# Optimization experiments

Hardware: AMD Instinct MI355X
Metric: run time of the kernel (lower is better)

Reference implementation:

```python
import jax, jax.numpy as jnp
import numpy as np

NEG_SLOPE = 0.2  # PyG GATConv default leaky_relu negative slope

N_NODES = 10000
N_EDGES = 80000
IN_FEAT = 200
HID = 400
IN_HEADS = 8
OUT_FEAT = 200


def setup_inputs() -> dict:
    key = jax.random.key(0)
    ks = jax.random.split(key, 12)
    input_data = jax.random.normal(ks[0], (N_NODES, IN_FEAT), dtype=jnp.float32)
    edge_index = jax.random.randint(ks[1], (2, N_EDGES), 0, N_NODES, dtype=jnp.int64)
    # conv1: GATConv(200 -> 400, heads=8, concat=True)
    W1 = jax.random.normal(ks[2], (IN_FEAT, IN_HEADS * HID), dtype=jnp.float32) * 0.05
    a_src1 = jax.random.normal(ks[3], (IN_HEADS, HID), dtype=jnp.float32) * 0.05
    a_dst1 = jax.random.normal(ks[4], (IN_HEADS, HID), dtype=jnp.float32) * 0.05
    b1 = jnp.zeros((IN_HEADS * HID,), dtype=jnp.float32)
    # conv2: GATConv(3200 -> 200, heads=1, concat=False)
    W2 = jax.random.normal(ks[5], (IN_HEADS * HID, 1 * OUT_FEAT), dtype=jnp.float32) * 0.05
    a_src2 = jax.random.normal(ks[6], (1, OUT_FEAT), dtype=jnp.float32) * 0.05
    a_dst2 = jax.random.normal(ks[7], (1, OUT_FEAT), dtype=jnp.float32) * 0.05
    b2 = jnp.zeros((OUT_FEAT,), dtype=jnp.float32)
    return {"input_data": input_data, "edge_index": edge_index,
            "W1": W1, "a_src1": a_src1, "a_dst1": a_dst1, "b1": b1,
            "W2": W2, "a_src2": a_src2, "a_dst2": a_dst2, "b2": b2}


def _gat_conv(x, src, dst, W, a_src, a_dst, b, heads, out_ch, concat):
    """PyG GATConv (v1 attention), eval mode (no dropout)."""
    n = x.shape[0]
    h = (x @ W).reshape(n, heads, out_ch)              # [N,H,C]
    al_s = jnp.sum(h * a_src, axis=-1)                 # [N,H]
    al_d = jnp.sum(h * a_dst, axis=-1)                 # [N,H]
    e = jax.nn.leaky_relu(al_s[src] + al_d[dst], NEG_SLOPE)  # [E,H]
    # segment softmax over edges sharing the same destination node
    e_max = jax.ops.segment_max(e, dst, num_segments=n)       # [N,H]
    e_exp = jnp.exp(e - e_max[dst])                            # [E,H]
    denom = jax.ops.segment_sum(e_exp, dst, num_segments=n)   # [N,H]
    alpha = e_exp / denom[dst]                                 # [E,H]
    msg = h[src] * alpha[:, :, None]                           # [E,H,C]
    out = jax.ops.segment_sum(msg, dst, num_segments=n)       # [N,H,C]
    out = out.reshape(n, heads * out_ch) if concat else out.mean(axis=1)
    return out + b


def reference(input_data, edge_index, W1, a_src1, a_dst1, b1, W2, a_src2, a_dst2, b2):
    n = input_data.shape[0]
    loop = jnp.arange(n, dtype=edge_index.dtype)
    src = jnp.concatenate([edge_index[0], loop])  # add self-loops (PyG default)
    dst = jnp.concatenate([edge_index[1], loop])
    # eval mode: F.dropout is identity
    x = _gat_conv(input_data, src, dst, W1, a_src1, a_dst1, b1, IN_HEADS, HID, True)
    x = jax.nn.elu(x)
    x = _gat_conv(x, src, dst, W2, a_src2, a_dst2, b2, 1, OUT_FEAT, False)
    return x
```

## Files before the change

### kernel.cpp

```cpp
#include <hip/hip_runtime.h>
#include <math.h>

#define N_NODES 10000
#define N_EDGES 80000
#define ET (N_EDGES + N_NODES)
#define IN_FEAT 200
#define HID 400
#define NH1 8
#define F1 (NH1 * HID)
#define OUT_FEAT 200
#define NEG_SLOPE 0.2f

#define M_PAD 10048
#define K1 224
#define HSL (NH1 * K1)
#define XH_K 416
#define C1P 448
#define KALL (NH1 * XH_K)
#define N2P2 256
#define XHS 456

typedef __attribute__((ext_vector_type(8))) short short8_t;
typedef __attribute__((ext_vector_type(4))) float f32x4;


__device__ inline void edge_sd(const int* __restrict__ ei, int e, int& s, int& d) {
    if (e < N_EDGES) { s = ei[e]; d = ei[N_EDGES + e]; }
    else { s = e - N_EDGES; d = s; }
}

__device__ inline unsigned short f2bf(float x) {
    unsigned u = __float_as_uint(x);
    unsigned r = u + 0x7FFFu + ((u >> 16) & 1u);
    return (unsigned short)(r >> 16);
}

#define W1N (NH1 * C1P * K1)
#define W2N (N2P2 * KALL)
__global__ __launch_bounds__(256) void prep_w(const float* __restrict__ W1,
                                              const float* __restrict__ W2,
                                              unsigned short* __restrict__ W1f,
                                              unsigned short* __restrict__ W2f) {
    int idx = blockIdx.x * blockDim.x + threadIdx.x;
    if (idx < W1N) {
        int e    = idx & 7;
        int lane = (idx >> 3) & 63;
        int rem  = idx >> 9;
        int ks   = rem % 7;
        int jgh  = rem / 7;
        int jg   = jgh % 28;
        int h    = jgh / 28;
        int c = jg * 16 + (lane & 15);
        int k = ks * 32 + (lane >> 4) * 8 + e;
        float v = (k < IN_FEAT && c < HID) ? W1[(size_t)k * F1 + h * HID + c] : 0.f;
        W1f[idx] = f2bf(v);
    } else if (idx < W1N + W2N) {
        int t    = idx - W1N;
        int e    = t & 7;
        int lane = (t >> 3) & 63;
        int rem  = t >> 9;
        int ks   = rem % 13;
        int cgh  = rem / 13;
        int cg   = cgh % 16;
        int h    = cgh / 16;
        int c = cg * 16 + (lane & 15);
        int k = ks * 32 + (lane >> 4) * 8 + e;
        float v = (c < OUT_FEAT && k < HID) ? W2[(size_t)(h * HID + k) * OUT_FEAT + c] : 0.f;
        W2f[t] = f2bf(v);
    }
}

__global__ __launch_bounds__(256) void pvec_k(const float* __restrict__ W1,
                                              const float* __restrict__ a_src,
                                              const float* __restrict__ a_dst,
                                              float* __restrict__ p_src,
                                              float* __restrict__ p_dst) {
    int idx = blockIdx.x * blockDim.x + threadIdx.x;
    if (idx >= 2 * NH1 * IN_FEAT) return;
    int which = idx / (NH1 * IN_FEAT);
    int r = idx - which * (NH1 * IN_FEAT);
    int h = r / IN_FEAT, k = r - h * IN_FEAT;
    const float* av = (which == 0 ? a_src : a_dst) + h * HID;
    const float* wrow = W1 + (size_t)k * F1 + h * HID;
    float acc = 0.f;
    for (int c = 0; c < HID; ++c) acc += wrow[c] * av[c];
    (which == 0 ? p_src : p_dst)[h * IN_FEAT + k] = acc;
}

__global__ __launch_bounds__(512) void att1x(const float* __restrict__ X,
                                             const float* __restrict__ p_src,
                                             const float* __restrict__ p_dst,
                                             float* __restrict__ als,
                                             float* __restrict__ ald) {
    const int n    = blockIdx.x;
    const int head = threadIdx.x >> 6;
    const int lane = threadIdx.x & 63;
    const float* xp = X + (size_t)n * IN_FEAT;
    const float* ps = p_src + head * IN_FEAT;
    const float* pd = p_dst + head * IN_FEAT;
    float ss = 0.f, sd = 0.f;
    for (int k = lane; k < IN_FEAT; k += 64) {
        float v = xp[k];
        ss += v * ps[k];
        sd += v * pd[k];
    }
    for (int off = 32; off; off >>= 1) {
        ss += __shfl_down(ss, off);
        sd += __shfl_down(sd, off);
    }
    if (lane == 0) { als[n * NH1 + head] = ss; ald[n * NH1 + head] = sd; }
}

__global__ __launch_bounds__(256) void count_k(const int* __restrict__ ei, int* __restrict__ counts) {
    int e = blockIdx.x * blockDim.x + threadIdx.x;
    if (e >= ET) return;
    int s, d; edge_sd(ei, e, s, d);
    atomicAdd(&counts[d], 1);
}

__global__ __launch_bounds__(1024) void scan_k(const int* __restrict__ counts, int* __restrict__ offs) {
    __shared__ int part[1024];
    const int tid = threadIdx.x;
    const int base = tid * 10;
    int loc[10];
    int s = 0;
    for (int i = 0; i < 10; ++i) {
        int idx = base + i;
        int c = (idx < N_NODES) ? counts[idx] : 0;
        loc[i] = s; s += c;
    }
    part[tid] = s;
    __syncthreads();
    for (int off = 1; off < 1024; off <<= 1) {
        int v = (tid >= off) ? part[tid - off] : 0;
        __syncthreads();
        part[tid] += v;
        __syncthreads();
    }
    int pre = (tid > 0) ? part[tid - 1] : 0;
    for (int i = 0; i < 10; ++i) {
        int idx = base + i;
        if (idx < N_NODES) offs[idx] = pre + loc[i];
    }
    if (tid == 1023) offs[N_NODES] = part[1023];
}

__global__ __launch_bounds__(256) void scatter_k(const int* __restrict__ ei,
                                                 const int* __restrict__ offs,
                                                 int* __restrict__ cursor,
                                                 int* __restrict__ esrc) {
    int e = blockIdx.x * blockDim.x + threadIdx.x;
    if (e >= ET) return;
    int s, d; edge_sd(ei, e, s, d);
    int pos = atomicAdd(&cursor[d], 1);
    esrc[offs[d] + pos] = s;
}

__global__ __launch_bounds__(512) void agg1x(const float* __restrict__ X,
                                             const float* __restrict__ als1,
                                             const float* __restrict__ ald1,
                                             const int* __restrict__ offs,
                                             const int* __restrict__ esrc,
                                             unsigned short* __restrict__ xaggb) {
    __shared__ unsigned short sb[8][HSL];
    const int wave = threadIdx.x >> 6;
    const int lane = threadIdx.x & 63;
    const int n = blockIdx.x * 8 + wave;

    if (n < N_NODES) {
        float acc[NH1][4];
#pragma unroll
        for (int h = 0; h < NH1; ++h)
#pragma unroll
            for (int g = 0; g < 4; ++g) acc[h][g] = 0.f;

        const int beg = offs[n], end = offs[n + 1];
        float aldv = 0.f, m = -INFINITY, l = 0.f;
        if (lane < NH1) aldv = ald1[n * NH1 + lane];

        for (int t = beg; t < end; ++t) {
            const int s = esrc[t];
            if (lane < NH1) {
                float v = als1[s * NH1 + lane] + aldv;
                v = v > 0.f ? v : NEG_SLOPE * v;
                float mn = fmaxf(m, v);
                l = l * __expf(m - mn) + __expf(v - mn);
                m = mn;
            }
        }
        const float inv_l = (lane < NH1) ? 1.f / l : 0.f;

        for (int t = beg; t < end; ++t) {
            const int s = esrc[t];
            float aval = 0.f;
            if (lane < NH1) {
                float v = als1[s * NH1 + lane] + aldv;
                v = v > 0.f ? v : NEG_SLOPE * v;
                aval = __expf(v - m) * inv_l;
            }
            const float* xp = X + (size_t)s * IN_FEAT;
            float x0 = xp[lane];
            float x1 = xp[64 + lane];
            float x2 = xp[128 + lane];
            float x3 = (lane < 8) ? xp[192 + lane] : 0.f;
#pragma unroll
            for (int h = 0; h < NH1; ++h) {
                float a = __shfl(aval, h);
                acc[h][0] += a * x0;
                acc[h][1] += a * x1;
                acc[h][2] += a * x2;
                acc[h][3] += a * x3;
            }
        }
#pragma unroll
        for (int h = 0; h < NH1; ++h) {
            sb[wave][h * K1 + lane]        = f2bf(acc[h][0]);
            sb[wave][h * K1 + 64 + lane]   = f2bf(acc[h][1]);
            sb[wave][h * K1 + 128 + lane]  = f2bf(acc[h][2]);
            if (lane < 32) {
                unsigned short v3 = (lane < 8) ? f2bf(acc[h][3]) : (unsigned short)0;
                sb[wave][h * K1 + 192 + lane] = v3;
            }
        }
    } else {
        for (int j = lane; j < HSL; j += 64) sb[wave][j] = 0;
    }
    __syncthreads();
    const uint4* s4 = (const uint4*)(&sb[0][0]);
    uint4* d4 = (uint4*)(xaggb + (size_t)blockIdx.x * 8 * HSL);
    for (int c = threadIdx.x; c < 8 * HSL / 8; c += 512) d4[c] = s4[c];
}

__global__ __launch_bounds__(256, 2) void fused_gemm(const unsigned short* __restrict__ xaggb,
                                                     const unsigned short* __restrict__ W1f,
                                                     const float* __restrict__ b1,
                                                     const unsigned short* __restrict__ W2f,
                                                     float* __restrict__ h2p) {
    __shared__ unsigned short xhf[16 * XHS];
    const int wave = threadIdx.x >> 6;
    const int lane = threadIdx.x & 63;
    const int row  = lane & 15;
    const int kg   = lane >> 4;
    const int h    = blockIdx.y;
    const int m0   = blockIdx.x * 16;
    const int c0   = wave * 112;
    const int c2   = wave * 64;

    const unsigned short* ap = xaggb + (size_t)(m0 + row) * HSL + h * K1 + kg * 8;
    short8_t areg[7];
#pragma unroll
    for (int ks = 0; ks < 7; ++ks)
        areg[ks] = *(const short8_t*)(ap + ks * 32);

    const unsigned short* w1h = W1f + (((size_t)h * 28 + wave * 7) * 7) * 512 + lane * 8;
    f32x4 acc[7];
#pragma unroll
    for (int j = 0; j < 7; ++j) acc[j] = (f32x4){0.f, 0.f, 0.f, 0.f};
#pragma unroll
    for (int ks = 0; ks < 7; ++ks) {
        short8_t b[7];
#pragma unroll
        for (int j = 0; j < 7; ++j)
            b[j] = *(const short8_t*)(w1h + (size_t)(j * 7 + ks) * 512);
#pragma unroll
        for (int j = 0; j < 7; ++j)
            acc[j] = __builtin_amdgcn_mfma_f32_16x16x32_bf16(areg[ks], b[j], acc[j], 0, 0, 0);
    }

#pragma unroll
    for (int j = 0; j < 7; ++j) {
        int cc = c0 + j * 16 + row;
        float bias = (cc < HID) ? b1[h * HID + cc] : 0.f;
#pragma unroll
        for (int r = 0; r < 4; ++r) {
            int rl = kg * 4 + r;
            float v = acc[j][r] + bias;
            v = v > 0.f ? v : (__expf(v) - 1.f);
            xhf[rl * XHS + cc] = f2bf(v);
        }
    }
    __syncthreads();

    const unsigned short* w2h = W2f + (((size_t)h * 16 + wave * 4) * 13) * 512 + lane * 8;
    f32x4 oacc[4];
#pragma unroll
    for (int j = 0; j < 4; ++j) oacc[j] = (f32x4){0.f, 0.f, 0.f, 0.f};
#pragma unroll
    for (int ks = 0; ks < 13; ++ks) {
        short8_t b[4];
#pragma unroll
        for (int j = 0; j < 4; ++j)
            b[j] = *(const short8_t*)(w2h + (size_t)(j * 13 + ks) * 512);
        short8_t a = *(const short8_t*)&xhf[row * XHS + ks * 32 + kg * 8];
#pragma unroll
        for (int j = 0; j < 4; ++j)
            oacc[j] = __builtin_amdgcn_mfma_f32_16x16x32_bf16(a, b[j], oacc[j], 0, 0, 0);
    }

    float* op = h2p + ((size_t)h * M_PAD + (m0 + kg * 4)) * OUT_FEAT;
#pragma unroll
    for (int j = 0; j < 4; ++j) {
        int cc = c2 + j * 16 + row;
        if (cc < OUT_FEAT) {
#pragma unroll
            for (int r = 0; r < 4; ++r)
                op[(size_t)r * OUT_FEAT + cc] = oacc[j][r];
        }
    }
}

__global__ __launch_bounds__(256) void reduce_att2(const float* __restrict__ h2p,
                                                   const float* __restrict__ a_src,
                                                   const float* __restrict__ a_dst,
                                                   float* __restrict__ h2,
                                                   float* __restrict__ als,
                                                   float* __restrict__ ald) {
    const int wave = threadIdx.x >> 6;
    const int lane = threadIdx.x & 63;
    const int row  = blockIdx.x * 4 + wave;

    f32x4 sum = {0.f, 0.f, 0.f, 0.f};
    if (lane < 50) {
        const float* p = h2p + (size_t)row * OUT_FEAT + lane * 4;
#pragma unroll
        for (int h = 0; h < NH1; ++h)
            sum += *(const f32x4*)(p + (size_t)h * M_PAD * OUT_FEAT);
        *(f32x4*)(h2 + (size_t)row * OUT_FEAT + lane * 4) = sum;
    }
    float ss = 0.f, sd = 0.f;
    if (lane < 50) {
        f32x4 as = *(const f32x4*)(a_src + lane * 4);
        f32x4 ad = *(const f32x4*)(a_dst + lane * 4);
#pragma unroll
        for (int j = 0; j < 4; ++j) { ss += sum[j] * as[j]; sd += sum[j] * ad[j]; }
    }
    for (int off = 32; off; off >>= 1) {
        ss += __shfl_down(ss, off);
        sd += __shfl_down(sd, off);
    }
    if (lane == 0 && row < N_NODES) { als[row] = ss; ald[row] = sd; }
}

__global__ __launch_bounds__(256) void agg2_csr(const float* __restrict__ h2,
                                                const float* __restrict__ als2,
                                                const float* __restrict__ ald2,
                                                const int* __restrict__ offs,
                                                const int* __restrict__ esrc,
                                                const float* __restrict__ b2,
                                                float* __restrict__ out) {
    const int n = blockIdx.x;
    const int k = threadIdx.x;
    const float aldn = ald2[n];
    const int beg = offs[n], end = offs[n + 1];

    float m = -INFINITY, l = 0.f;
    for (int t = beg; t < end; ++t) {
        int s = esrc[t];
        float v = als2[s] + aldn;
        v = v > 0.f ? v : NEG_SLOPE * v;
        float mn = fmaxf(m, v);
        l = l * __expf(m - mn) + __expf(v - mn);
        m = mn;
    }
    const float inv_l = 1.f / l;

    if (k >= OUT_FEAT) return;
    float acc = 0.f;
    for (int t = beg; t < end; ++t) {
        int s = esrc[t];
        float v = als2[s] + aldn;
        v = v > 0.f ? v : NEG_SLOPE * v;
        float a = __expf(v - m) * inv_l;
        acc += a * h2[(size_t)s * OUT_FEAT + k];
    }
    out[(size_t)n * OUT_FEAT + k] = acc + b2[k];
}

extern "C" void kernel_launch(void* const* d_in, const int* in_sizes, int n_in,
                              void* d_out, int out_size, void* d_ws, size_t ws_size,
                              hipStream_t stream) {
    const float* X   = (const float*)d_in[0];
    const int*   ei  = (const int*)d_in[1];
    const float* W1  = (const float*)d_in[2];
    const float* as1 = (const float*)d_in[3];
    const float* ad1 = (const float*)d_in[4];
    const float* b1  = (const float*)d_in[5];
    const float* W2  = (const float*)d_in[6];
    const float* as2 = (const float*)d_in[7];
    const float* ad2 = (const float*)d_in[8];
    const float* b2  = (const float*)d_in[9];
    float* out = (float*)d_out;

    char* base = (char*)d_ws;
    auto carve = [&](size_t bytes) -> void* {
        void* p = (void*)base;
        base += (bytes + 255) & ~(size_t)255;
        return p;
    };
    float* p_src1 = (float*)carve(NH1 * IN_FEAT * 4);
    float* p_dst1 = (float*)carve(NH1 * IN_FEAT * 4);
    float* als1   = (float*)carve(N_NODES * NH1 * 4);
    float* ald1   = (float*)carve(N_NODES * NH1 * 4);
    float* als2   = (float*)carve(N_NODES * 4);
    float* ald2   = (float*)carve(N_NODES * 4);
    float* h2     = (float*)carve((size_t)M_PAD * OUT_FEAT * 4);
    int* counts   = (int*)carve(N_NODES * 4);
    int* cursor   = (int*)carve(N_NODES * 4);
    int* offs     = (int*)carve((N_NODES + 1) * 4);
    int* esrc     = (int*)carve(ET * 4);
    unsigned short* xaggb = (unsigned short*)carve((size_t)M_PAD * HSL * 2);
    unsigned short* W1f   = (unsigned short*)carve((size_t)W1N * 2);
    unsigned short* W2f   = (unsigned short*)carve((size_t)W2N * 2);
    float* h2p    = (float*)carve((size_t)NH1 * M_PAD * OUT_FEAT * 4);

    hipMemsetAsync(counts, 0, 2 * 40192, stream);

    count_k<<<(ET + 255) / 256, 256, 0, stream>>>(ei, counts);
    scan_k<<<1, 1024, 0, stream>>>(counts, offs);
    scatter_k<<<(ET + 255) / 256, 256, 0, stream>>>(ei, offs, cursor, esrc);
    prep_w<<<(W1N + W2N + 255) / 256, 256, 0, stream>>>(W1, W2, W1f, W2f);
    pvec_k<<<(2 * NH1 * IN_FEAT + 255) / 256, 256, 0, stream>>>(W1, as1, ad1, p_src1, p_dst1);
    att1x<<<N_NODES, 512, 0, stream>>>(X, p_src1, p_dst1, als1, ald1);

    agg1x<<<M_PAD / 8, 512, 0, stream>>>(X, als1, ald1, offs, esrc, xaggb);

    fused_gemm<<<dim3(M_PAD / 16, NH1), 256, 0, stream>>>(xaggb, W1f, b1, W2f, h2p);

    reduce_att2<<<M_PAD / 4, 256, 0, stream>>>(h2p, as2, ad2, h2, als2, ald2);

    agg2_csr<<<N_NODES, 256, 0, stream>>>(h2, als2, ald2, offs, esrc, b2, out);
}
```

Baseline: 257.3 us.

## Parallelize softmax stats across lanes and fuse two heads per GEMM block

```diff
diff --git a/kernel.cpp b/kernel.cpp
--- a/kernel.cpp
+++ b/kernel.cpp
@@ -19,6 +19,7 @@
 #define KALL (NH1 * XH_K)
 #define N2P2 256
 #define XHS 456
+#define NQ 4
 
 typedef __attribute__((ext_vector_type(8))) short short8_t;
 typedef __attribute__((ext_vector_type(4))) float f32x4;
@@ -33,6 +34,13 @@
     unsigned u = __float_as_uint(x);
     unsigned r = u + 0x7FFFu + ((u >> 16) & 1u);
     return (unsigned short)(r >> 16);
+}
+
+__device__ inline void sm_merge(float& m, float& l, float m2, float l2) {
+    float mn = fmaxf(m, m2);
+    float t1 = (m  > -1e30f) ? l  * __expf(m  - mn) : 0.f;
+    float t2 = (m2 > -1e30f) ? l2 * __expf(m2 - mn) : 0.f;
+    m = mn; l = t1 + t2;
 }
 
 #define W1N (NH1 * C1P * K1)
@@ -175,20 +183,26 @@
             for (int g = 0; g < 4; ++g) acc[h][g] = 0.f;
 
         const int beg = offs[n], end = offs[n + 1];
-        float aldv = 0.f, m = -INFINITY, l = 0.f;
-        if (lane < NH1) aldv = ald1[n * NH1 + lane];
-
-        for (int t = beg; t < end; ++t) {
+        const int grp = lane >> 3;
+        const int hd  = lane & 7;
+        const float aldv = ald1[n * NH1 + hd];
+
+        float m = -INFINITY, l = 0.f;
+        for (int t = beg + grp; t < end; t += 8) {
             const int s = esrc[t];
-            if (lane < NH1) {
-                float v = als1[s * NH1 + lane] + aldv;
-                v = v > 0.f ? v : NEG_SLOPE * v;
-                float mn = fmaxf(m, v);
-                l = l * __expf(m - mn) + __expf(v - mn);
-                m = mn;
-            }
-        }
-        const float inv_l = (lane < NH1) ? 1.f / l : 0.f;
+            float v = als1[s * NH1 + hd] + aldv;
+            v = v > 0.f ? v : NEG_SLOPE * v;
+            float mn = fmaxf(m, v);
+            l = l * __expf(m - mn) + __expf(v - mn);
+            m = mn;
+        }
+#pragma unroll
+        for (int off = 8; off < 64; off <<= 1) {
+            float m2 = __shfl_xor(m, off);
+            float l2 = __shfl_xor(l, off);
+            sm_merge(m, l, m2, l2);
+        }
+        const float inv_l = 1.f / l;
 
         for (int t = beg; t < end; ++t) {
             const int s = esrc[t];
@@ -241,63 +255,69 @@
     const int lane = threadIdx.x & 63;
     const int row  = lane & 15;
     const int kg   = lane >> 4;
-    const int h    = blockIdx.y;
     const int m0   = blockIdx.x * 16;
     const int c0   = wave * 112;
     const int c2   = wave * 64;
 
-    const unsigned short* ap = xaggb + (size_t)(m0 + row) * HSL + h * K1 + kg * 8;
-    short8_t areg[7];
-#pragma unroll
-    for (int ks = 0; ks < 7; ++ks)
-        areg[ks] = *(const short8_t*)(ap + ks * 32);
-
-    const unsigned short* w1h = W1f + (((size_t)h * 28 + wave * 7) * 7) * 512 + lane * 8;
-    f32x4 acc[7];
-#pragma unroll
-    for (int j = 0; j < 7; ++j) acc[j] = (f32x4){0.f, 0.f, 0.f, 0.f};
-#pragma unroll
-    for (int ks = 0; ks < 7; ++ks) {
-        short8_t b[7];
-#pragma unroll
-        for (int j = 0; j < 7; ++j)
-            b[j] = *(const short8_t*)(w1h + (size_t)(j * 7 + ks) * 512);
-#pragma unroll
-        for (int j = 0; j < 7; ++j)
-            acc[j] = __builtin_amdgcn_mfma_f32_16x16x32_bf16(areg[ks], b[j], acc[j], 0, 0, 0);
-    }
-
-#pragma unroll
-    for (int j = 0; j < 7; ++j) {
-        int cc = c0 + j * 16 + row;
-        float bias = (cc < HID) ? b1[h * HID + cc] : 0.f;
-#pragma unroll
-        for (int r = 0; r < 4; ++r) {
-            int rl = kg * 4 + r;
-            float v = acc[j][r] + bias;
-            v = v > 0.f ? v : (__expf(v) - 1.f);
-            xhf[rl * XHS + cc] = f2bf(v);
-        }
-    }
-    __syncthreads();
-
-    const unsigned short* w2h = W2f + (((size_t)h * 16 + wave * 4) * 13) * 512 + lane * 8;
     f32x4 oacc[4];
 #pragma unroll
     for (int j = 0; j < 4; ++j) oacc[j] = (f32x4){0.f, 0.f, 0.f, 0.f};
-#pragma unroll
-    for (int ks = 0; ks < 13; ++ks) {
-        short8_t b[4];
-#pragma unroll
-        for (int j = 0; j < 4; ++j)
-            b[j] = *(const short8_t*)(w2h + (size_t)(j * 13 + ks) * 512);
-        short8_t a = *(const short8_t*)&xhf[row * XHS + ks * 32 + kg * 8];
-#pragma unroll
-        for (int j = 0; j < 4; ++j)
-            oacc[j] = __builtin_amdgcn_mfma_f32_16x16x32_bf16(a, b[j], oacc[j], 0, 0, 0);
-    }
-
-    float* op = h2p + ((size_t)h * M_PAD + (m0 + kg * 4)) * OUT_FEAT;
+
+#pragma unroll
+    for (int hh = 0; hh < 2; ++hh) {
+        const int h = blockIdx.y * 2 + hh;
+        if (hh > 0) __syncthreads();
+
+        const unsigned short* ap = xaggb + (size_t)(m0 + row) * HSL + h * K1 + kg * 8;
+        short8_t areg[7];
+#pragma unroll
+        for (int ks = 0; ks < 7; ++ks)
+            areg[ks] = *(const short8_t*)(ap + ks * 32);
+
+        const unsigned short* w1h = W1f + (((size_t)h * 28 + wave * 7) * 7) * 512 + lane * 8;
+        f32x4 acc[7];
+#pragma unroll
+        for (int j = 0; j < 7; ++j) acc[j] = (f32x4){0.f, 0.f, 0.f, 0.f};
+#pragma unroll
+        for (int ks = 0; ks < 7; ++ks) {
+            short8_t b[7];
+#pragma unroll
+            for (int j = 0; j < 7; ++j)
+                b[j] = *(const short8_t*)(w1h + (size_t)(j * 7 + ks) * 512);
+#pragma unroll
+            for (int j = 0; j < 7; ++j)
+                acc[j] = __builtin_amdgcn_mfma_f32_16x16x32_bf16(areg[ks], b[j], acc[j], 0, 0, 0);
+        }
+
+#pragma unroll
+        for (int j = 0; j < 7; ++j) {
+            int cc = c0 + j * 16 + row;
+            float bias = (cc < HID) ? b1[h * HID + cc] : 0.f;
+#pragma unroll
+            for (int r = 0; r < 4; ++r) {
+                int rl = kg * 4 + r;
+                float v = acc[j][r] + bias;
+                v = v > 0.f ? v : (__expf(v) - 1.f);
+                xhf[rl * XHS + cc] = f2bf(v);
+            }
+        }
+        __syncthreads();
+
+        const unsigned short* w2h = W2f + (((size_t)h * 16 + wave * 4) * 13) * 512 + lane * 8;
+#pragma unroll
+        for (int ks = 0; ks < 13; ++ks) {
+            short8_t b[4];
+#pragma unroll
+            for (int j = 0; j < 4; ++j)
+                b[j] = *(const short8_t*)(w2h + (size_t)(j * 13 + ks) * 512);
+            short8_t a = *(const short8_t*)&xhf[row * XHS + ks * 32 + kg * 8];
+#pragma unroll
+            for (int j = 0; j < 4; ++j)
+                oacc[j] = __builtin_amdgcn_mfma_f32_16x16x32_bf16(a, b[j], oacc[j], 0, 0, 0);
+        }
+    }
+
+    float* op = h2p + ((size_t)blockIdx.y * M_PAD + (m0 + kg * 4)) * OUT_FEAT;
 #pragma unroll
     for (int j = 0; j < 4; ++j) {
         int cc = c2 + j * 16 + row;
@@ -323,8 +343,8 @@
     if (lane < 50) {
         const float* p = h2p + (size_t)row * OUT_FEAT + lane * 4;
 #pragma unroll
-        for (int h = 0; h < NH1; ++h)
-            sum += *(const f32x4*)(p + (size_t)h * M_PAD * OUT_FEAT);
+        for (int q = 0; q < NQ; ++q)
+            sum += *(const f32x4*)(p + (size_t)q * M_PAD * OUT_FEAT);
         *(f32x4*)(h2 + (size_t)row * OUT_FEAT + lane * 4) = sum;
     }
     float ss = 0.f, sd = 0.f;
@@ -348,21 +368,32 @@
                                                 const int* __restrict__ esrc,
                                                 const float* __restrict__ b2,
                                                 float* __restrict__ out) {
+    __shared__ float sm, sl;
     const int n = blockIdx.x;
     const int k = threadIdx.x;
     const float aldn = ald2[n];
     const int beg = offs[n], end = offs[n + 1];
 
-    float m = -INFINITY, l = 0.f;
-    for (int t = beg; t < end; ++t) {
-        int s = esrc[t];
-        float v = als2[s] + aldn;
-        v = v > 0.f ? v : NEG_SLOPE * v;
-        float mn = fmaxf(m, v);
-        l = l * __expf(m - mn) + __expf(v - mn);
-        m = mn;
-    }
-    const float inv_l = 1.f / l;
+    if (k < 64) {
+        float m = -INFINITY, l = 0.f;
+        for (int t = beg + k; t < end; t += 64) {
+            int s = esrc[t];
+            float v = als2[s] + aldn;
+            v = v > 0.f ? v : NEG_SLOPE * v;
+            float mn = fmaxf(m, v);
+            l = l * __expf(m - mn) + __expf(v - mn);
+            m = mn;
+        }
+#pragma unroll
+        for (int off = 1; off < 64; off <<= 1) {
+            float m2 = __shfl_xor(m, off);
+            float l2 = __shfl_xor(l, off);
+            sm_merge(m, l, m2, l2);
+        }
+        if (k == 0) { sm = m; sl = 1.f / l; }
+    }
+    __syncthreads();
+    const float m = sm, inv_l = sl;
 
     if (k >= OUT_FEAT) return;
     float acc = 0.f;
@@ -411,7 +442,7 @@
     unsigned short* xaggb = (unsigned short*)carve((size_t)M_PAD * HSL * 2);
     unsigned short* W1f   = (unsigned short*)carve((size_t)W1N * 2);
     unsigned short* W2f   = (unsigned short*)carve((size_t)W2N * 2);
-    float* h2p    = (float*)carve((size_t)NH1 * M_PAD * OUT_FEAT * 4);
+    float* h2p    = (float*)carve((size_t)NQ * M_PAD * OUT_FEAT * 4);
 
     hipMemsetAsync(counts, 0, 2 * 40192, stream);
 
@@ -424,7 +455,7 @@
 
     agg1x<<<M_PAD / 8, 512, 0, stream>>>(X, als1, ald1, offs, esrc, xaggb);
 
-    fused_gemm<<<dim3(M_PAD / 16, NH1), 256, 0, stream>>>(xaggb, W1f, b1, W2f, h2p);
+    fused_gemm<<<dim3(M_PAD / 16, NQ), 256, 0, stream>>>(xaggb, W1f, b1, W2f, h2p);
 
     reduce_att2<<<M_PAD / 4, 256, 0, stream>>>(h2p, as2, ad2, h2, als2, ald2);
 
```

Result: faster. 236.7 us (-8.0%).
